# Kernel optimization log

Measured on AMD Instinct MI355X. Metric: run time of the kernel, lower is better.

The kernel has to match this reference:

```python
import jax, jax.numpy as jnp
import numpy as np

NH = 16      # num_attention_heads
NKV = 8      # num_key_value_heads
G = NH // NKV  # num_key_value_groups
D = 128      # head_dim = hidden_size // NH
ROPE_MAX = 2048


def _rope_tables(seq_len, dtype=jnp.float32):
    # matches RotaryEmbedding: inv_freq over even dims, freqs duplicated (concat), cos/sin cached
    inv_freq = 1.0 / (10000.0 ** (jnp.arange(0, D, 2, dtype=jnp.float32) / D))
    t = jnp.arange(ROPE_MAX, dtype=jnp.float32)[:, None]          # [max, 1]
    freqs = t * inv_freq[None, :]                                  # [max, D/2]
    freqs = jnp.concatenate((freqs, freqs), axis=-1)               # [max, D]
    cos = jnp.cos(freqs)[:seq_len].astype(dtype)                   # [S, D]
    sin = jnp.sin(freqs)[:seq_len].astype(dtype)
    # unsqueeze(0) then unsqueeze(2) -> [1, S, 1, D] broadcasting over batch and heads
    return cos[None, :, None, :], sin[None, :, None, :]


def _rotate_half(x):
    x1, x2 = jnp.split(x, 2, axis=-1)
    return jnp.concatenate((-x2, x1), axis=-1)


def setup_inputs() -> dict:
    key = jax.random.key(0)
    ks = jax.random.split(key, 5)
    B, S, H = 2, 2048, 2048
    scale = 1.0 / np.sqrt(H)
    return {
        "hidden_states": jax.random.normal(ks[0], (B, S, H), jnp.float32),
        "Wq": jax.random.normal(ks[1], (H, H), jnp.float32) * scale,
        "Wk": jax.random.normal(ks[2], (NKV * D, H), jnp.float32) * scale,
        "Wv": jax.random.normal(ks[3], (NKV * D, H), jnp.float32) * scale,
        "Wo": jax.random.normal(ks[4], (H, H), jnp.float32) * scale,
    }


def reference(hidden_states, Wq, Wk, Wv, Wo):
    B, S, H = hidden_states.shape
    # projections (nn.Linear: y = x @ W.T, no bias)
    q = (hidden_states @ Wq.T).reshape(B, S, NH, D)     # [B,S,NH,D]
    k = (hidden_states @ Wk.T).reshape(B, S, NKV, D)    # [B,S,NKV,D]
    v = (hidden_states @ Wv.T).reshape(B, S, NKV, D)

    cos, sin = _rope_tables(S, hidden_states.dtype)
    q = q * cos + _rotate_half(q) * sin
    k = k * cos + _rotate_half(k) * sin

    # GQA: query head h attends to kv head h // G (repeat_kv ordering: h = n*G + g)
    qg = q.reshape(B, S, NKV, G, D).transpose(0, 2, 3, 1, 4)   # [B,NKV,G,S,D]
    kt = k.transpose(0, 2, 1, 3)                                # [B,NKV,S,D]
    vt = v.transpose(0, 2, 1, 3)                                # [B,NKV,S,D]

    scores = jnp.einsum("bngqd,bnkd->bngqk", qg, kt) / np.sqrt(D)  # [B,NKV,G,S,S]
    causal = jnp.triu(jnp.ones((S, S), dtype=bool), k=1)
    neg = jnp.finfo(scores.dtype).min
    scores = jnp.where(causal[None, None, None], neg, scores)
    probs = jax.nn.softmax(scores.astype(jnp.float32), axis=-1).astype(q.dtype)

    out = jnp.einsum("bngqk,bnkd->bngqd", probs, vt)            # [B,NKV,G,S,D]
    out = out.transpose(0, 3, 1, 2, 4).reshape(B, S, H)         # [B,S,H]
    return out @ Wo.T
```

## Files before the change

### kernel.cpp

```cpp
#include <hip/hip_runtime.h>

typedef unsigned short u16;
typedef __attribute__((ext_vector_type(8))) short short8;
typedef __attribute__((ext_vector_type(4))) float f32x4;

__device__ __forceinline__ u16 f2bf(float f) {
  unsigned u = __float_as_uint(f);
  return (u16)((u + 0x7FFFu + ((u >> 16) & 1u)) >> 16);
}
__device__ __forceinline__ float bf2f(u16 h) {
  return __uint_as_float(((unsigned)h) << 16);
}
__device__ __forceinline__ unsigned cvt_pk_bf16(float lo, float hi) {
  unsigned r;
  asm("v_cvt_pk_bf16_f32 %0, %1, %2" : "=v"(r) : "v"(lo), "v"(hi));
  return r;
}

__device__ __forceinline__ void gload_lds16(const void* g, void* l) {
  __builtin_amdgcn_global_load_lds(
      (const __attribute__((address_space(1))) unsigned*)g,
      (__attribute__((address_space(3))) unsigned*)l, 16, 0, 0);
}

__global__ void cast_f32_bf16_k(const float4* __restrict__ in, u16* __restrict__ out, int n4) {
  int i = blockIdx.x * 256 + threadIdx.x;
  if (i >= n4) return;
  float4 v = in[i];
  union { u16 u[4]; uint2 d; } r;
  r.u[0] = f2bf(v.x); r.u[1] = f2bf(v.y); r.u[2] = f2bf(v.z); r.u[3] = f2bf(v.w);
  *reinterpret_cast<uint2*>(out + (size_t)i * 4) = r.d;
}

__global__ void rope_tables_k(float* __restrict__ cosT, float* __restrict__ sinT) {
  int idx = blockIdx.x * 256 + threadIdx.x;
  int i = idx & 63, s = idx >> 6;
  double inv = pow(10000.0, -(double)(2 * i) / 128.0);
  double f = (double)s * inv;
  cosT[idx] = (float)cos(f);
  sinT[idx] = (float)sin(f);
}

__global__ void rope_q_k(u16* __restrict__ x, const float* __restrict__ cosT,
                         const float* __restrict__ sinT) {
  int idx = blockIdx.x * 256 + threadIdx.x;
  int i = idx & 63;
  int hh = (idx >> 6) & 15;
  int row = idx >> 10;
  int s = row & 2047;
  size_t base = (size_t)row * 4096 + hh * 128;
  float x1 = bf2f(x[base + i]);
  float x2 = bf2f(x[base + i + 64]);
  float c = cosT[s * 64 + i], sn = sinT[s * 64 + i];
  x[base + i]      = f2bf(x1 * c - x2 * sn);
  x[base + i + 64] = f2bf(x2 * c + x1 * sn);
}

__global__ void rope_repack_k_k(const u16* __restrict__ qkv, u16* __restrict__ kt,
                                const float* __restrict__ cosT, const float* __restrict__ sinT) {
  int idx = blockIdx.x * 256 + threadIdx.x;
  int i = idx & 63;
  int kvh = (idx >> 6) & 7;
  int row = idx >> 9;
  int s = row & 2047, b = row >> 11;
  size_t src = (size_t)row * 4096 + 2048 + kvh * 128;
  float x1 = bf2f(qkv[src + i]);
  float x2 = bf2f(qkv[src + i + 64]);
  float c = cosT[s * 64 + i], sn = sinT[s * 64 + i];
  size_t dst = ((size_t)(b * 8 + kvh) * 2048 + s) * 128;
  kt[dst + i]      = f2bf(x1 * c - x2 * sn);
  kt[dst + i + 64] = f2bf(x2 * c + x1 * sn);
}

__global__ void transpose_v_k(const u16* __restrict__ qkv, u16* __restrict__ vt) {
  __shared__ u16 tile[128][129];
  int bn = blockIdx.y;
  int s0 = blockIdx.x * 128;
  int b = bn >> 3, n = bn & 7;
  for (int e = threadIdx.x; e < 128 * 128; e += 256) {
    int r = e >> 7, c = e & 127;
    tile[r][c] = qkv[(size_t)(b * 2048 + s0 + r) * 4096 + 3072 + n * 128 + c];
  }
  __syncthreads();
  for (int e = threadIdx.x; e < 128 * 128; e += 256) {
    int r = e >> 7, c = e & 127;
    vt[((size_t)bn * 128 + r) * 2048 + s0 + c] = tile[c][r];
  }
}

template<typename OutT>
__global__ __launch_bounds__(512, 1) void gemm256p_k(
    const u16* __restrict__ A, const u16* __restrict__ Bm,
    OutT* __restrict__ C, int M, int N, int K)
{
  __shared__ __align__(16) u16 As[2][2][256 * 32];
  __shared__ __align__(16) u16 Bs[2][2][256 * 32];
  const int tid = threadIdx.x;
  const int wave = tid >> 6, lane = tid & 63;
  const int wm = wave >> 2, wn = wave & 3;
  const int lrow = lane & 15, lgrp = lane >> 4;
  const int gx = (int)gridDim.x;
  const int nwg = gx * (int)gridDim.y;
  const int f = (int)(blockIdx.y * gridDim.x + blockIdx.x);
  const int sw = (f & 7) * (nwg >> 3) + (f >> 3);
  const int bx = sw % gx, by = sw / gx;
  const int row0 = by * 256, col0 = bx * 256;

  f32x4 acc[8][4];
  #pragma unroll
  for (int m = 0; m < 8; ++m)
    #pragma unroll
    for (int n = 0; n < 4; ++n) acc[m][n] = (f32x4){0.f, 0.f, 0.f, 0.f};

  const int NT = K >> 6;
  const int psw = lgrp ^ (lrow & 3);

  auto stageA = [&](int buf, int t, int ks) {
    const int k0 = (t << 6) + ks * 32;
    #pragma unroll
    for (int i = 0; i < 2; ++i) {
      int s = i * 512 + tid;
      int row = s >> 2, p = s & 3;
      int g = p ^ (row & 3);
      gload_lds16(A + (size_t)(row0 + row) * K + k0 + g * 8,
                  &As[buf][ks][(size_t)(i * 512 + wave * 64) * 8]);
    }
  };
  auto stageB = [&](int buf, int t, int ks) {
    const int k0 = (t << 6) + ks * 32;
    #pragma unroll
    for (int i = 0; i < 2; ++i) {
      int s = i * 512 + tid;
      int row = s >> 2, p = s & 3;
      int g = p ^ (row & 3);
      gload_lds16(Bm + (size_t)(col0 + row) * K + k0 + g * 8,
                  &Bs[buf][ks][(size_t)(i * 512 + wave * 64) * 8]);
    }
  };

  stageA(0, 0, 0); stageB(0, 0, 0); stageA(0, 0, 1); stageB(0, 0, 1);

  for (int t = 0; t < NT; ++t) {
    const int cur = t & 1, nxt = cur ^ 1;
    const bool pf = (t + 1 < NT);
    short8 af[4], bfr[4];

    if (pf) { stageA(nxt, t + 1, 0); asm volatile("s_waitcnt vmcnt(6)" ::: "memory"); }
    else    {                        asm volatile("s_waitcnt vmcnt(4)" ::: "memory"); }
    __builtin_amdgcn_s_barrier();
    __builtin_amdgcn_sched_barrier(0);
    #pragma unroll
    for (int m = 0; m < 4; ++m)
      af[m] = *reinterpret_cast<const short8*>(&As[cur][0][(wm * 128 + m * 16 + lrow) * 32 + psw * 8]);
    #pragma unroll
    for (int n = 0; n < 4; ++n)
      bfr[n] = *reinterpret_cast<const short8*>(&Bs[cur][0][(wn * 64 + n * 16 + lrow) * 32 + psw * 8]);
    asm volatile("s_waitcnt lgkmcnt(0)" ::: "memory");
    __builtin_amdgcn_sched_barrier(0);
    __builtin_amdgcn_s_setprio(1);
    #pragma unroll
    for (int m = 0; m < 4; ++m)
      #pragma unroll
      for (int n = 0; n < 4; ++n)
        acc[m][n] = __builtin_amdgcn_mfma_f32_16x16x32_bf16(af[m], bfr[n], acc[m][n], 0, 0, 0);
    __builtin_amdgcn_s_setprio(0);

    if (pf) stageB(nxt, t + 1, 0);
    #pragma unroll
    for (int m = 0; m < 4; ++m)
      af[m] = *reinterpret_cast<const short8*>(&As[cur][0][(wm * 128 + (m + 4) * 16 + lrow) * 32 + psw * 8]);
    asm volatile("s_waitcnt lgkmcnt(0)" ::: "memory");
    __builtin_amdgcn_sched_barrier(0);
    __builtin_amdgcn_s_setprio(1);
    #pragma unroll
    for (int m = 0; m < 4; ++m)
      #pragma unroll
      for (int n = 0; n < 4; ++n)
        acc[m + 4][n] = __builtin_amdgcn_mfma_f32_16x16x32_bf16(af[m], bfr[n], acc[m + 4][n], 0, 0, 0);
    __builtin_amdgcn_s_setprio(0);

    if (pf) { stageA(nxt, t + 1, 1); asm volatile("s_waitcnt vmcnt(6)" ::: "memory"); }
    else    {                        asm volatile("s_waitcnt vmcnt(0)" ::: "memory"); }
    __builtin_amdgcn_s_barrier();
    __builtin_amdgcn_sched_barrier(0);
    #pragma unroll
    for (int m = 0; m < 4; ++m)
      af[m] = *reinterpret_cast<const short8*>(&As[cur][1][(wm * 128 + m * 16 + lrow) * 32 + psw * 8]);
    #pragma unroll
    for (int n = 0; n < 4; ++n)
      bfr[n] = *reinterpret_cast<const short8*>(&Bs[cur][1][(wn * 64 + n * 16 + lrow) * 32 + psw * 8]);
    asm volatile("s_waitcnt lgkmcnt(0)" ::: "memory");
    __builtin_amdgcn_sched_barrier(0);
    __builtin_amdgcn_s_setprio(1);
    #pragma unroll
    for (int m = 0; m < 4; ++m)
      #pragma unroll
      for (int n = 0; n < 4; ++n)
        acc[m][n] = __builtin_amdgcn_mfma_f32_16x16x32_bf16(af[m], bfr[n], acc[m][n], 0, 0, 0);
    __builtin_amdgcn_s_setprio(0);

    if (pf) stageB(nxt, t + 1, 1);
    #pragma unroll
    for (int m = 0; m < 4; ++m)
      af[m] = *reinterpret_cast<const short8*>(&As[cur][1][(wm * 128 + (m + 4) * 16 + lrow) * 32 + psw * 8]);
    asm volatile("s_waitcnt lgkmcnt(0)" ::: "memory");
    __builtin_amdgcn_sched_barrier(0);
    __builtin_amdgcn_s_setprio(1);
    #pragma unroll
    for (int m = 0; m < 4; ++m)
      #pragma unroll
      for (int n = 0; n < 4; ++n)
        acc[m + 4][n] = __builtin_amdgcn_mfma_f32_16x16x32_bf16(af[m], bfr[n], acc[m + 4][n], 0, 0, 0);
    __builtin_amdgcn_s_setprio(0);
  }

  #pragma unroll
  for (int m = 0; m < 8; ++m)
    #pragma unroll
    for (int n = 0; n < 4; ++n)
      #pragma unroll
      for (int j = 0; j < 4; ++j) {
        int r = row0 + wm * 128 + m * 16 + lgrp * 4 + j;
        int col = col0 + wn * 64 + n * 16 + lrow;
        float val = acc[m][n][j];
        if constexpr (sizeof(OutT) == 2) C[(size_t)r * N + col] = f2bf(val);
        else                             C[(size_t)r * N + col] = val;
      }
}

template<typename OutT, int BN>
__global__ __launch_bounds__(512, 1) void gemm256_k(
    const u16* __restrict__ A, const u16* __restrict__ Bm,
    OutT* __restrict__ C, int M, int N, int K)
{
  constexpr int BITER = (BN * 8) / 512;
  constexpr int NFR = BN / 64;
  __shared__ __align__(16) u16 As[2][256 * 64];
  __shared__ __align__(16) u16 Bs[2][BN * 64];
  const int tid = threadIdx.x;
  const int wave = tid >> 6, lane = tid & 63;
  const int wm = wave >> 2, wn = wave & 3;
  const int lrow = lane & 15, lgrp = lane >> 4;
  const int gx = (int)gridDim.x;
  const int nwg = gx * (int)gridDim.y;
  const int f = (int)(blockIdx.y * gridDim.x + blockIdx.x);
  const int sw = (f & 7) * (nwg >> 3) + (f >> 3);
  const int bx = sw % gx, by = sw / gx;
  const int row0 = by * 256, col0 = bx * BN;

  f32x4 acc[8][NFR];
  #pragma unroll
  for (int m = 0; m < 8; ++m)
    #pragma unroll
    for (int n = 0; n < NFR; ++n) acc[m][n] = (f32x4){0.f, 0.f, 0.f, 0.f};

  const int NT = K >> 6;

  auto stage = [&](int buf, int k0) {
    #pragma unroll
    for (int i = 0; i < 4; ++i) {
      int cid = i * 512 + tid;
      int row = cid >> 3, cp = cid & 7;
      int c = cp ^ (row & 7);
      gload_lds16(A + (size_t)(row0 + row) * K + k0 + c * 8,
                  &As[buf][(size_t)(i * 512 + wave * 64) * 8]);
    }
    #pragma unroll
    for (int i = 0; i < BITER; ++i) {
      int cid = i * 512 + tid;
      int row = cid >> 3, cp = cid & 7;
      int c = cp ^ (row & 7);
      gload_lds16(Bm + (size_t)(col0 + row) * K + k0 + c * 8,
                  &Bs[buf][(size_t)(i * 512 + wave * 64) * 8]);
    }
  };

  stage(0, 0);
  for (int t = 0; t < NT; ++t) {
    const int cur = t & 1;
    if (t + 1 < NT) {
      stage(cur ^ 1, (t + 1) << 6);
      if constexpr (BN == 256) asm volatile("s_waitcnt vmcnt(8)" ::: "memory");
      else                     asm volatile("s_waitcnt vmcnt(6)" ::: "memory");
    } else {
      asm volatile("s_waitcnt vmcnt(0)" ::: "memory");
    }
    __builtin_amdgcn_s_barrier();
    __builtin_amdgcn_sched_barrier(0);
    #pragma unroll
    for (int ks = 0; ks < 2; ++ks) {
      short8 af[8], bfr[NFR];
      #pragma unroll
      for (int m = 0; m < 8; ++m) {
        int row = wm * 128 + m * 16 + lrow;
        int cp = (ks * 4 + lgrp) ^ (row & 7);
        af[m] = *reinterpret_cast<const short8*>(&As[cur][row * 64 + cp * 8]);
      }
      #pragma unroll
      for (int n = 0; n < NFR; ++n) {
        int row = wn * (NFR * 16) + n * 16 + lrow;
        int cp = (ks * 4 + lgrp) ^ (row & 7);
        bfr[n] = *reinterpret_cast<const short8*>(&Bs[cur][row * 64 + cp * 8]);
      }
      #pragma unroll
      for (int m = 0; m < 8; ++m)
        #pragma unroll
        for (int n = 0; n < NFR; ++n)
          acc[m][n] = __builtin_amdgcn_mfma_f32_16x16x32_bf16(af[m], bfr[n], acc[m][n], 0, 0, 0);
    }
    __builtin_amdgcn_sched_barrier(0);
    __builtin_amdgcn_s_barrier();
  }

  #pragma unroll
  for (int m = 0; m < 8; ++m)
    #pragma unroll
    for (int n = 0; n < NFR; ++n)
      #pragma unroll
      for (int j = 0; j < 4; ++j) {
        int r = row0 + wm * 128 + m * 16 + lgrp * 4 + j;
        int col = col0 + wn * (NFR * 16) + n * 16 + lrow;
        float val = acc[m][n][j];
        if constexpr (sizeof(OutT) == 2) C[(size_t)r * N + col] = f2bf(val);
        else                             C[(size_t)r * N + col] = val;
      }
}

__global__ __launch_bounds__(256, 2) void flash_attn_k(
    const u16* __restrict__ qkv, const u16* __restrict__ kt,
    const u16* __restrict__ vt, u16* __restrict__ o)
{
  constexpr int S = 2048, NH = 16, NKV = 8, D = 128;
  const int wave = threadIdx.x >> 6, lane = threadIdx.x & 63;
  const int flat = blockIdx.x;
  const int pr = flat >> 5;
  const int bh = (flat & 7) * 4 + ((flat >> 3) & 3);
  const int b = bh >> 4, h = bh & 15;
  const int kvh = h >> 1;
  const int lrow = lane & 15, lgrp = lane >> 4;

  __shared__ __align__(16) u16 ks[2][64 * 128];
  __shared__ __align__(16) u16 vs[2][128 * 64];

  const float scl2 = 0.12754245006443634f;
  const u16* khead = kt + (size_t)(b * NKV + kvh) * S * D;
  const u16* vhead = vt + (size_t)(b * NKV + kvh) * D * S;

  const int srcA = lrow + 16 * ((2 * lgrp) & 3);
  const int srcB = srcA + 16;
  const bool hiSel = (lgrp >= 2);

  auto stage = [&](int nxt, int kv0n) {
    #pragma unroll
    for (int i = 0; i < 4; ++i) {
      int c = i * 256 + wave * 64 + lane;
      int kr = c >> 4;
      int kc16 = (c & 15) ^ (kr & 7);
      gload_lds16(khead + (size_t)(kv0n + kr) * D + kc16 * 8,
                  &ks[nxt][(size_t)(i * 256 + wave * 64) * 8]);
      int vr = c >> 3;
      int vc = (c & 7) ^ (vr & 7);
      gload_lds16(vhead + (size_t)vr * S + kv0n + vc * 8,
                  &vs[nxt][(size_t)(i * 256 + wave * 64) * 8]);
    }
  };

  #pragma unroll
  for (int ph = 0; ph < 2; ++ph) {
    const int qt = ph ? pr : (31 - pr);
    const int q0 = qt * 64 + wave * 16;
    const int trips = qt + 1;

    short8 qf[4];
    const u16* qbase = qkv + (size_t)(b * S + q0 + lrow) * 4096 + h * 128;
    #pragma unroll
    for (int kc = 0; kc < 4; ++kc)
      qf[kc] = *reinterpret_cast<const short8*>(qbase + kc * 32 + lgrp * 8);

    f32x4 acc[8];
    #pragma unroll
    for (int n = 0; n < 8; ++n) acc[n] = (f32x4){0.f, 0.f, 0.f, 0.f};
    float l_part = 0.f;

    stage(0, 0);

    for (int t = 0; t < trips; ++t) {
      const int cur = t & 1;
      asm volatile("s_waitcnt vmcnt(0)" ::: "memory");
      __builtin_amdgcn_s_barrier();
      __builtin_amdgcn_sched_barrier(0);
      f32x4 sc[4];
      #pragma unroll
      for (int nb = 0; nb < 4; ++nb) {
        sc[nb] = (f32x4){0.f, 0.f, 0.f, 0.f};
        const int r = nb * 16 + lrow;
        #pragma unroll
        for (int kc = 0; kc < 4; ++kc) {
          int ch = (kc * 4 + lgrp) ^ (r & 7);
          short8 kf = *reinterpret_cast<const short8*>(&ks[cur][r * 128 + ch * 8]);
          sc[nb] = __builtin_amdgcn_mfma_f32_16x16x32_bf16(kf, qf[kc], sc[nb], 0, 0, 0);
        }
      }
      if (t + 1 < trips) stage(cur ^ 1, (t + 1) * 64);
      float p[4][4];
      if (t < trips - 1) {
        #pragma unroll
        for (int nb = 0; nb < 4; ++nb)
          #pragma unroll
          for (int j = 0; j < 4; ++j)
            p[nb][j] = exp2f(fminf(sc[nb][j] * scl2, 43.f));
      } else {
        #pragma unroll
        for (int nb = 0; nb < 4; ++nb) {
          if (nb < wave) {
            #pragma unroll
            for (int j = 0; j < 4; ++j)
              p[nb][j] = exp2f(fminf(sc[nb][j] * scl2, 43.f));
          } else if (nb == wave) {
            #pragma unroll
            for (int j = 0; j < 4; ++j)
              p[nb][j] = (lgrp * 4 + j <= lrow) ? exp2f(fminf(sc[nb][j] * scl2, 43.f)) : 0.f;
          } else {
            #pragma unroll
            for (int j = 0; j < 4; ++j) p[nb][j] = 0.f;
          }
        }
      }
      #pragma unroll
      for (int nb = 0; nb < 4; ++nb)
        #pragma unroll
        for (int j = 0; j < 4; ++j) l_part += p[nb][j];
      unsigned pk[4][2];
      #pragma unroll
      for (int nb = 0; nb < 4; ++nb) {
        pk[nb][0] = cvt_pk_bf16(p[nb][0], p[nb][1]);
        pk[nb][1] = cvt_pk_bf16(p[nb][2], p[nb][3]);
      }
      short8 pfB[2];
      #pragma unroll
      for (int half = 0; half < 2; ++half) {
        unsigned lo0 = __shfl(pk[2 * half][0], srcA), hi0 = __shfl(pk[2 * half + 1][0], srcA);
        unsigned lo1 = __shfl(pk[2 * half][1], srcA), hi1 = __shfl(pk[2 * half + 1][1], srcA);
        unsigned lo2 = __shfl(pk[2 * half][0], srcB), hi2 = __shfl(pk[2 * half + 1][0], srcB);
        unsigned lo3 = __shfl(pk[2 * half][1], srcB), hi3 = __shfl(pk[2 * half + 1][1], srcB);
        union { unsigned u[4]; short8 s8; } asm_u;
        asm_u.u[0] = hiSel ? hi0 : lo0;
        asm_u.u[1] = hiSel ? hi1 : lo1;
        asm_u.u[2] = hiSel ? hi2 : lo2;
        asm_u.u[3] = hiSel ? hi3 : lo3;
        pfB[half] = asm_u.s8;
      }
      #pragma unroll
      for (int n = 0; n < 8; ++n) {
        const int d = n * 16 + lrow;
        #pragma unroll
        for (int kc2 = 0; kc2 < 2; ++kc2) {
          int ch = (kc2 * 4 + lgrp) ^ (d & 7);
          short8 vf = *reinterpret_cast<const short8*>(&vs[cur][d * 64 + ch * 8]);
          acc[n] = __builtin_amdgcn_mfma_f32_16x16x32_bf16(vf, pfB[kc2], acc[n], 0, 0, 0);
        }
      }
    }

    float s = l_part;
    s += __shfl_xor(s, 16);
    s += __shfl_xor(s, 32);
    float inv = 1.f / s;
    u16* obase = o + (((size_t)(b * S + q0 + lrow)) * NH + h) * D;
    #pragma unroll
    for (int n = 0; n < 8; ++n) {
      uint2 wv;
      wv.x = cvt_pk_bf16(acc[n][0] * inv, acc[n][1] * inv);
      wv.y = cvt_pk_bf16(acc[n][2] * inv, acc[n][3] * inv);
      *reinterpret_cast<uint2*>(obase + n * 16 + lgrp * 4) = wv;
    }
    __syncthreads();
  }
}

extern "C" void kernel_launch(void* const* d_in, const int* in_sizes, int n_in,
                              void* d_out, int out_size, void* d_ws, size_t ws_size,
                              hipStream_t stream) {
  const float* hs = (const float*)d_in[0];
  const float* Wq = (const float*)d_in[1];
  const float* Wk = (const float*)d_in[2];
  const float* Wv = (const float*)d_in[3];
  const float* Wo = (const float*)d_in[4];
  float* out = (float*)d_out;

  constexpr int B = 2, S = 2048, H = 2048, NH = 16, NKV = 8, D = 128;
  constexpr int M = B * S;
  constexpr int NQKV = 4096;

  char* w = (char*)d_ws;
  auto alloc = [&](size_t bytes) { char* p = w; w += (bytes + 255) & ~(size_t)255; return p; };
  u16* hs_bf   = (u16*)alloc((size_t)M * H * 2);
  u16* wqkv_bf = (u16*)alloc((size_t)NQKV * H * 2);
  u16* wo_bf   = (u16*)alloc((size_t)H * H * 2);
  u16* qkv     = (u16*)alloc((size_t)M * NQKV * 2);
  float* cosT  = (float*)alloc((size_t)S * 64 * 4);
  float* sinT  = (float*)alloc((size_t)S * 64 * 4);
  u16* attn = hs_bf;
  u16* vt   = wqkv_bf;
  u16* kt   = wqkv_bf + (size_t)B * NKV * D * S;

  cast_f32_bf16_k<<<(M * H / 4) / 256, 256, 0, stream>>>((const float4*)hs, hs_bf, M * H / 4);
  cast_f32_bf16_k<<<(H * H / 4) / 256, 256, 0, stream>>>((const float4*)Wq, wqkv_bf, H * H / 4);
  cast_f32_bf16_k<<<(NKV * D * H / 4) / 256, 256, 0, stream>>>((const float4*)Wk, wqkv_bf + (size_t)2048 * H, NKV * D * H / 4);
  cast_f32_bf16_k<<<(NKV * D * H / 4) / 256, 256, 0, stream>>>((const float4*)Wv, wqkv_bf + (size_t)3072 * H, NKV * D * H / 4);
  cast_f32_bf16_k<<<(H * H / 4) / 256, 256, 0, stream>>>((const float4*)Wo, wo_bf, H * H / 4);
  rope_tables_k<<<(S * 64) / 256, 256, 0, stream>>>(cosT, sinT);

  gemm256p_k<u16><<<dim3(NQKV / 256, M / 256), 512, 0, stream>>>(hs_bf, wqkv_bf, qkv, M, NQKV, H);

  rope_q_k<<<(M * 16 * 64) / 256, 256, 0, stream>>>(qkv, cosT, sinT);
  rope_repack_k_k<<<(M * 8 * 64) / 256, 256, 0, stream>>>(qkv, kt, cosT, sinT);
  transpose_v_k<<<dim3(S / 128, B * NKV), 256, 0, stream>>>(qkv, vt);

  flash_attn_k<<<512, 256, 0, stream>>>(qkv, kt, vt, attn);

  gemm256_k<float, 128><<<dim3(H / 128, M / 256), 512, 0, stream>>>(attn, wo_bf, out, M, H, H);
}
```

Before: 230.6 us.

## Restructure GEMM staging to full 64-wide K tiles and hoist attention prefetch

```diff
diff --git a/kernel.cpp b/kernel.cpp
--- a/kernel.cpp
+++ b/kernel.cpp
@@ -93,8 +93,8 @@
     const u16* __restrict__ A, const u16* __restrict__ Bm,
     OutT* __restrict__ C, int M, int N, int K)
 {
-  __shared__ __align__(16) u16 As[2][2][256 * 32];
-  __shared__ __align__(16) u16 Bs[2][2][256 * 32];
+  __shared__ __align__(16) u16 As[2][256 * 64];
+  __shared__ __align__(16) u16 Bs[2][256 * 64];
   const int tid = threadIdx.x;
   const int wave = tid >> 6, lane = tid & 63;
   const int wm = wave >> 2, wn = wave & 3;
@@ -113,48 +113,49 @@
     for (int n = 0; n < 4; ++n) acc[m][n] = (f32x4){0.f, 0.f, 0.f, 0.f};
 
   const int NT = K >> 6;
-  const int psw = lgrp ^ (lrow & 3);
-
-  auto stageA = [&](int buf, int t, int ks) {
-    const int k0 = (t << 6) + ks * 32;
-    #pragma unroll
-    for (int i = 0; i < 2; ++i) {
-      int s = i * 512 + tid;
-      int row = s >> 2, p = s & 3;
-      int g = p ^ (row & 3);
-      gload_lds16(A + (size_t)(row0 + row) * K + k0 + g * 8,
-                  &As[buf][ks][(size_t)(i * 512 + wave * 64) * 8]);
+
+  auto stage = [&](int buf, int k0) {
+    #pragma unroll
+    for (int i = 0; i < 4; ++i) {
+      int cid = i * 512 + tid;
+      int row = cid >> 3, cp = cid & 7;
+      int c = cp ^ (row & 7);
+      gload_lds16(A + (size_t)(row0 + row) * K + k0 + c * 8,
+                  &As[buf][(size_t)(i * 512 + wave * 64) * 8]);
+    }
+    #pragma unroll
+    for (int i = 0; i < 4; ++i) {
+      int cid = i * 512 + tid;
+      int row = cid >> 3, cp = cid & 7;
+      int c = cp ^ (row & 7);
+      gload_lds16(Bm + (size_t)(col0 + row) * K + k0 + c * 8,
+                  &Bs[buf][(size_t)(i * 512 + wave * 64) * 8]);
     }
   };
-  auto stageB = [&](int buf, int t, int ks) {
-    const int k0 = (t << 6) + ks * 32;
-    #pragma unroll
-    for (int i = 0; i < 2; ++i) {
-      int s = i * 512 + tid;
-      int row = s >> 2, p = s & 3;
-      int g = p ^ (row & 3);
-      gload_lds16(Bm + (size_t)(col0 + row) * K + k0 + g * 8,
-                  &Bs[buf][ks][(size_t)(i * 512 + wave * 64) * 8]);
-    }
-  };
-
-  stageA(0, 0, 0); stageB(0, 0, 0); stageA(0, 0, 1); stageB(0, 0, 1);
-
+
+  stage(0, 0);
   for (int t = 0; t < NT; ++t) {
     const int cur = t & 1, nxt = cur ^ 1;
-    const bool pf = (t + 1 < NT);
     short8 af[4], bfr[4];
 
-    if (pf) { stageA(nxt, t + 1, 0); asm volatile("s_waitcnt vmcnt(6)" ::: "memory"); }
-    else    {                        asm volatile("s_waitcnt vmcnt(4)" ::: "memory"); }
+    if (t + 1 < NT) {
+      stage(nxt, (t + 1) << 6);
+      asm volatile("s_waitcnt vmcnt(8)" ::: "memory");
+    } else {
+      asm volatile("s_waitcnt vmcnt(0)" ::: "memory");
+    }
     __builtin_amdgcn_s_barrier();
     __builtin_amdgcn_sched_barrier(0);
     #pragma unroll
-    for (int m = 0; m < 4; ++m)
-      af[m] = *reinterpret_cast<const short8*>(&As[cur][0][(wm * 128 + m * 16 + lrow) * 32 + psw * 8]);
-    #pragma unroll
-    for (int n = 0; n < 4; ++n)
-      bfr[n] = *reinterpret_cast<const short8*>(&Bs[cur][0][(wn * 64 + n * 16 + lrow) * 32 + psw * 8]);
+    for (int m = 0; m < 4; ++m) {
+      int row = wm * 128 + m * 16 + lrow;
+      af[m] = *reinterpret_cast<const short8*>(&As[cur][row * 64 + (lgrp ^ (row & 7)) * 8]);
+    }
+    #pragma unroll
+    for (int n = 0; n < 4; ++n) {
+      int row = wn * 64 + n * 16 + lrow;
+      bfr[n] = *reinterpret_cast<const short8*>(&Bs[cur][row * 64 + (lgrp ^ (row & 7)) * 8]);
+    }
     asm volatile("s_waitcnt lgkmcnt(0)" ::: "memory");
     __builtin_amdgcn_sched_barrier(0);
     __builtin_amdgcn_s_setprio(1);
@@ -165,10 +166,11 @@
         acc[m][n] = __builtin_amdgcn_mfma_f32_16x16x32_bf16(af[m], bfr[n], acc[m][n], 0, 0, 0);
     __builtin_amdgcn_s_setprio(0);
 
-    if (pf) stageB(nxt, t + 1, 0);
-    #pragma unroll
-    for (int m = 0; m < 4; ++m)
-      af[m] = *reinterpret_cast<const short8*>(&As[cur][0][(wm * 128 + (m + 4) * 16 + lrow) * 32 + psw * 8]);
+    #pragma unroll
+    for (int m = 0; m < 4; ++m) {
+      int row = wm * 128 + (m + 4) * 16 + lrow;
+      af[m] = *reinterpret_cast<const short8*>(&As[cur][row * 64 + (lgrp ^ (row & 7)) * 8]);
+    }
     asm volatile("s_waitcnt lgkmcnt(0)" ::: "memory");
     __builtin_amdgcn_sched_barrier(0);
     __builtin_amdgcn_s_setprio(1);
@@ -179,16 +181,16 @@
         acc[m + 4][n] = __builtin_amdgcn_mfma_f32_16x16x32_bf16(af[m], bfr[n], acc[m + 4][n], 0, 0, 0);
     __builtin_amdgcn_s_setprio(0);
 
-    if (pf) { stageA(nxt, t + 1, 1); asm volatile("s_waitcnt vmcnt(6)" ::: "memory"); }
-    else    {                        asm volatile("s_waitcnt vmcnt(0)" ::: "memory"); }
-    __builtin_amdgcn_s_barrier();
-    __builtin_amdgcn_sched_barrier(0);
-    #pragma unroll
-    for (int m = 0; m < 4; ++m)
-      af[m] = *reinterpret_cast<const short8*>(&As[cur][1][(wm * 128 + m * 16 + lrow) * 32 + psw * 8]);
-    #pragma unroll
-    for (int n = 0; n < 4; ++n)
-      bfr[n] = *reinterpret_cast<const short8*>(&Bs[cur][1][(wn * 64 + n * 16 + lrow) * 32 + psw * 8]);
+    #pragma unroll
+    for (int m = 0; m < 4; ++m) {
+      int row = wm * 128 + m * 16 + lrow;
+      af[m] = *reinterpret_cast<const short8*>(&As[cur][row * 64 + ((4 + lgrp) ^ (row & 7)) * 8]);
+    }
+    #pragma unroll
+    for (int n = 0; n < 4; ++n) {
+      int row = wn * 64 + n * 16 + lrow;
+      bfr[n] = *reinterpret_cast<const short8*>(&Bs[cur][row * 64 + ((4 + lgrp) ^ (row & 7)) * 8]);
+    }
     asm volatile("s_waitcnt lgkmcnt(0)" ::: "memory");
     __builtin_amdgcn_sched_barrier(0);
     __builtin_amdgcn_s_setprio(1);
@@ -199,10 +201,11 @@
         acc[m][n] = __builtin_amdgcn_mfma_f32_16x16x32_bf16(af[m], bfr[n], acc[m][n], 0, 0, 0);
     __builtin_amdgcn_s_setprio(0);
 
-    if (pf) stageB(nxt, t + 1, 1);
-    #pragma unroll
-    for (int m = 0; m < 4; ++m)
-      af[m] = *reinterpret_cast<const short8*>(&As[cur][1][(wm * 128 + (m + 4) * 16 + lrow) * 32 + psw * 8]);
+    #pragma unroll
+    for (int m = 0; m < 4; ++m) {
+      int row = wm * 128 + (m + 4) * 16 + lrow;
+      af[m] = *reinterpret_cast<const short8*>(&As[cur][row * 64 + ((4 + lgrp) ^ (row & 7)) * 8]);
+    }
     asm volatile("s_waitcnt lgkmcnt(0)" ::: "memory");
     __builtin_amdgcn_sched_barrier(0);
     __builtin_amdgcn_s_setprio(1);
@@ -212,6 +215,9 @@
       for (int n = 0; n < 4; ++n)
         acc[m + 4][n] = __builtin_amdgcn_mfma_f32_16x16x32_bf16(af[m], bfr[n], acc[m + 4][n], 0, 0, 0);
     __builtin_amdgcn_s_setprio(0);
+
+    __builtin_amdgcn_sched_barrier(0);
+    __builtin_amdgcn_s_barrier();
   }
 
   #pragma unroll
@@ -389,6 +395,7 @@
       asm volatile("s_waitcnt vmcnt(0)" ::: "memory");
       __builtin_amdgcn_s_barrier();
       __builtin_amdgcn_sched_barrier(0);
+      if (t + 1 < trips) stage(cur ^ 1, (t + 1) * 64);
       f32x4 sc[4];
       #pragma unroll
       for (int nb = 0; nb < 4; ++nb) {
@@ -401,7 +408,6 @@
           sc[nb] = __builtin_amdgcn_mfma_f32_16x16x32_bf16(kf, qf[kc], sc[nb], 0, 0, 0);
         }
       }
-      if (t + 1 < trips) stage(cur ^ 1, (t + 1) * 64);
       float p[4][4];
       if (t < trips - 1) {
         #pragma unroll
```

After: 236.6 us. +2.6%, slower.
